# Performance work log

Hardware: AMD Instinct MI355X
Metric: run time of the kernel (lower is better)

## Reference

```python
import jax, jax.numpy as jnp
import numpy as np
from jax import lax


def _conv(x, w, b, pad):
    # NCHW conv with OIHW weights, stride 1, symmetric padding.
    y = lax.conv_general_dilated(
        x, w, window_strides=(1, 1), padding=[(pad, pad), (pad, pad)],
        dimension_numbers=("NCHW", "OIHW", "NCHW"))
    return y + b[None, :, None, None]


def setup_inputs() -> dict:
    key = jax.random.key(0)
    ks = jax.random.split(key, 12)
    B, H, W = 8, 96, 128
    CORR = 324  # 4 * (2*4+1)^2
    return {
        "flow": jax.random.normal(ks[0], (B, 2, H, W), jnp.float32),
        "corr": jax.random.normal(ks[1], (B, CORR, H, W), jnp.float32),
        "wc1": jax.random.normal(ks[2], (256, CORR, 1, 1), jnp.float32) * 0.05,
        "bc1": jax.random.normal(ks[3], (256,), jnp.float32) * 0.05,
        "wc2": jax.random.normal(ks[4], (192, 256, 3, 3), jnp.float32) * 0.05,
        "bc2": jax.random.normal(ks[5], (192,), jnp.float32) * 0.05,
        "wf1": jax.random.normal(ks[6], (128, 2, 7, 7), jnp.float32) * 0.05,
        "bf1": jax.random.normal(ks[7], (128,), jnp.float32) * 0.05,
        "wf2": jax.random.normal(ks[8], (64, 128, 3, 3), jnp.float32) * 0.05,
        "bf2": jax.random.normal(ks[9], (64,), jnp.float32) * 0.05,
        "wo": jax.random.normal(ks[10], (126, 256, 3, 3), jnp.float32) * 0.05,
        "bo": jax.random.normal(ks[11], (126,), jnp.float32) * 0.05,
    }


def reference(flow, corr, wc1, bc1, wc2, bc2, wf1, bf1, wf2, bf2, wo, bo):
    # All DeformConv2d layers run with zero offsets -> standard convs.
    cor = jax.nn.relu(_conv(corr, wc1, bc1, 0))        # [B,256,H,W]
    cor = jax.nn.relu(_conv(cor, wc2, bc2, 1))         # [B,192,H,W]
    flo = jax.nn.relu(_conv(flow, wf1, bf1, 3))        # [B,128,H,W]
    flo = jax.nn.relu(_conv(flo, wf2, bf2, 1))         # [B,64,H,W]
    cor_flo = jnp.concatenate([cor, flo], axis=1)      # [B,256,H,W]
    out = jax.nn.relu(_conv(cor_flo, wo, bo, 1))       # [B,126,H,W]
    return jnp.concatenate([out, flow], axis=1)        # [B,128,H,W]
```

## Files before the change

kernel.cpp:

```cpp
#include <hip/hip_runtime.h>


typedef __bf16 bf16x8 __attribute__((ext_vector_type(8)));
typedef float f32x4 __attribute__((ext_vector_type(4)));

__device__ __forceinline__ unsigned short f2bf(float f) {
  __bf16 h = (__bf16)f;
  return __builtin_bit_cast(unsigned short, h);
}
__device__ __forceinline__ float bf2f(unsigned short u) {
  __bf16 h = __builtin_bit_cast(__bf16, u);
  return (float)h;
}

__device__ __forceinline__ void gload_lds16(const unsigned short* g,
                                            unsigned short* l) {
  __builtin_amdgcn_global_load_lds(
      (const __attribute__((address_space(1))) unsigned int*)g,
      (__attribute__((address_space(3))) unsigned int*)l, 16, 0, 0);
}

__global__ __launch_bounds__(256) void repack_w_bf16(
    const float* __restrict__ w, unsigned short* __restrict__ dst, int O, int I,
    int K2, int ICQ, int OCP) {
  int n = K2 * ICQ * OCP * 8;
  for (int s = blockIdx.x * 256 + threadIdx.x; s < n; s += gridDim.x * 256) {
    int j = s & 7;
    int r = s >> 3;
    int oc = r % OCP;
    r /= OCP;
    int icq = r % ICQ;
    int tap = r / ICQ;
    int ic = icq * 8 + j;
    float v = (oc < O && ic < I) ? w[((size_t)oc * I + ic) * K2 + tap] : 0.f;
    dst[s] = f2bf(v);
  }
}

__global__ __launch_bounds__(256) void repack_wf1(const float* __restrict__ w,
                                                  unsigned short* __restrict__ dst) {
  int s = blockIdx.x * 256 + threadIdx.x;
  if (s >= 16384) return;
  int j = s & 7;
  int oc = (s >> 3) & 127;
  int kq = s >> 10;
  int k = kq * 8 + j;
  float v = 0.f;
  if (k < 98) {
    int ic = k / 49;
    int tap = k - ic * 49;
    v = w[(oc * 2 + ic) * 49 + tap];
  }
  dst[s] = f2bf(v);
}

__global__ __launch_bounds__(256) void nchw2nhwc_bf16(
    const float* __restrict__ in, unsigned short* __restrict__ outp, int C,
    int CP, int HW) {
  __shared__ float sls[64][65];
  int p0 = blockIdx.x * 64;
  int c0 = blockIdx.y * 64;
  int b = p0 / HW, hw0 = p0 % HW;
  int tid = threadIdx.x;
  for (int e = tid; e < 4096; e += 256) {
    int ch = e >> 6, px = e & 63;
    float v = 0.f;
    if (c0 + ch < C) v = in[(size_t)(b * C + c0 + ch) * HW + hw0 + px];
    sls[px][ch] = v;
  }
  __syncthreads();
  for (int e = tid; e < 512; e += 256) {
    int px = e >> 3, cc = e & 7;
    if (c0 + cc * 8 < CP) {
      unsigned short pk[8];
#pragma unroll
      for (int j = 0; j < 8; ++j) pk[j] = f2bf(sls[px][cc * 8 + j]);
      *(uint4*)&outp[(size_t)(p0 + px) * CP + c0 + cc * 8] = *(uint4*)pk;
    }
  }
}

__global__ __launch_bounds__(256) void nhwc_bf16_2nchw(
    const unsigned short* __restrict__ inp, float* __restrict__ outp, int CP,
    int CO, int CT, int HW) {
  __shared__ float sls[64][65];
  int p0 = blockIdx.x * 64, c0 = blockIdx.y * 64;
  int b = p0 / HW, hw0 = p0 % HW;
  int tid = threadIdx.x;
  for (int e = tid; e < 512; e += 256) {
    int px = e >> 3, cc = e & 7;
    uint4 v = *(const uint4*)&inp[(size_t)(p0 + px) * CP + c0 + cc * 8];
    unsigned short* ps = (unsigned short*)&v;
#pragma unroll
    for (int j = 0; j < 8; ++j) sls[px][cc * 8 + j] = bf2f(ps[j]);
  }
  __syncthreads();
  for (int e = tid; e < 1024; e += 256) {
    int ch = e >> 4, pq = e & 15;
    if (c0 + ch < CO) {
      float4 v;
      v.x = sls[pq * 4 + 0][ch];
      v.y = sls[pq * 4 + 1][ch];
      v.z = sls[pq * 4 + 2][ch];
      v.w = sls[pq * 4 + 3][ch];
      *(float4*)&outp[(size_t)(b * CT + c0 + ch) * HW + hw0 + pq * 4] = v;
    }
  }
}

__global__ __launch_bounds__(256) void zero_halo3(unsigned short* b0,
                                                  unsigned short* b1,
                                                  unsigned short* b2) {
  unsigned short* buf = (blockIdx.y == 0) ? b0 : (blockIdx.y == 1) ? b1 : b2;
  const int C = (blockIdx.y == 2) ? 128 : 256;
  const int cq = C >> 3;
  int n = 8 * 452 * cq;
  int i = blockIdx.x * 256 + threadIdx.x;
  if (i >= n) return;
  int c = i % cq;
  int t = i / cq;
  int bp = t % 452;
  int bb = t / 452;
  int y, x;
  if (bp < 130) { y = 0; x = bp; }
  else if (bp < 260) { y = 97; x = bp - 130; }
  else { int r = bp - 260; y = 1 + (r >> 1); x = (r & 1) ? 129 : 0; }
  *(uint4*)&buf[((size_t)(bb * 98 + y) * 130 + x) * C + c * 8] =
      make_uint4(0, 0, 0, 0);
}

__global__ __launch_bounds__(256) void im2col_flow(const float* __restrict__ f,
                                                   unsigned short* __restrict__ o,
                                                   int H, int W) {
  int s = blockIdx.x * 256 + threadIdx.x;
  int kq = s & 15;
  int px = s >> 4;
  int HW = H * W;
  int b = px / HW;
  int r = px % HW;
  int y = r / W;
  int x = r % W;
  unsigned short pk[8];
#pragma unroll
  for (int j = 0; j < 8; ++j) {
    int k = kq * 8 + j;
    float v = 0.f;
    if (k < 98) {
      int ic = k / 49;
      int t = k - ic * 49;
      int dy = t / 7, dx = t - dy * 7;
      int yy = y + dy - 3, xx = x + dx - 3;
      if (yy >= 0 && yy < H && xx >= 0 && xx < W)
        v = f[((size_t)(b * 2 + ic) * H + yy) * W + xx];
    }
    pk[j] = f2bf(v);
  }
  *(uint4*)&o[(size_t)px * 128 + kq * 8] = *(uint4*)pk;
}

template <int CINP, int NF>
__global__ __launch_bounds__(256, 2) void mfma_gemm(
    const unsigned short* __restrict__ xin,
    const unsigned short* __restrict__ wpk,
    const float* __restrict__ bias, unsigned short* __restrict__ yout,
    int H, int W, int Cout, int OCP, int CT, int coff, int Wo, int oh) {
  __shared__ __align__(16) unsigned short smem[NF * 2048];
  const int tid = threadIdx.x;
  const int wave = tid >> 6, lane = tid & 63;
  const int l15 = lane & 15, lq = lane >> 4;
  const int tilesX = W >> 4;
  const int perB = (H >> 4) * tilesX;
  const int b = blockIdx.x / perB;
  const int r0 = blockIdx.x % perB;
  const int ty0 = (r0 / tilesX) << 4;
  const int tx0 = (r0 % tilesX) << 4;
  const int oc0 = blockIdx.y * (NF * 16);

  f32x4 acc[4][NF];
#pragma unroll
  for (int mf = 0; mf < 4; ++mf)
#pragma unroll
    for (int nf = 0; nf < NF; ++nf) acc[mf][nf] = (f32x4){0.f, 0.f, 0.f, 0.f};

  size_t rowA[4];
#pragma unroll
  for (int mf = 0; mf < 4; ++mf)
    rowA[mf] =
        ((size_t)(b * H + ty0 + wave * 4 + mf) * W + tx0 + l15) * CINP + lq * 8;
  const unsigned short* wB = wpk + ((size_t)lq * OCP + oc0 + l15) * 8;
  const int icbStr = 4 * OCP * 8;

  constexpr int NI = CINP / 32;
#pragma unroll 2
  for (int icb = 0; icb < NI; ++icb) {
    bf16x8 va[4], vb[NF];
#pragma unroll
    for (int mf = 0; mf < 4; ++mf)
      va[mf] = *(const bf16x8*)&xin[rowA[mf] + icb * 32];
#pragma unroll
    for (int nf = 0; nf < NF; ++nf)
      vb[nf] = *(const bf16x8*)&wB[icb * icbStr + nf * 128];
    __builtin_amdgcn_s_setprio(1);
#pragma unroll
    for (int mf = 0; mf < 4; ++mf)
#pragma unroll
      for (int nf = 0; nf < NF; ++nf)
        acc[mf][nf] = __builtin_amdgcn_mfma_f32_16x16x32_bf16(
            va[mf], vb[nf], acc[mf][nf], 0, 0, 0);
    __builtin_amdgcn_s_setprio(0);
  }

  float bsv[NF];
#pragma unroll
  for (int nf = 0; nf < NF; ++nf) {
    int oc = oc0 + nf * 16 + l15;
    bsv[nf] = (oc < Cout) ? bias[oc] : 0.f;
  }
  unsigned short* slice = smem + wave * (NF * 512);
  const int Ho = H + 2 * oh;
#pragma unroll
  for (int pass = 0; pass < 2; ++pass) {
#pragma unroll
    for (int mf = 0; mf < 4; ++mf)
#pragma unroll
      for (int h = 0; h < NF / 2; ++h) {
        const int nf = pass * (NF / 2) + h;
#pragma unroll
        for (int r = 0; r < 4; ++r)
          slice[(mf * 16 + lq * 4 + r) * (NF * 8) + h * 16 + l15] =
              f2bf(fmaxf(acc[mf][nf][r] + bsv[nf], 0.f));
      }
#pragma unroll
    for (int j = 0; j < NF; ++j) {
      int c = j * 64 + lane;
      int pxl = c / NF;
      int ocq = (c - pxl * NF) * 8;
      uint4 v = *(uint4*)&slice[pxl * (NF * 8) + ocq];
      int pxg = wave * 64 + pxl;
      int gy = ty0 + (pxg >> 4) + oh, gx = tx0 + (pxg & 15) + oh;
      *(uint4*)&yout[((size_t)(b * Ho + gy) * Wo + gx) * CT + coff + oc0 +
                     pass * (NF * 8) + ocq] = v;
    }
  }
}

template <int CINP, int NF>
__global__ __launch_bounds__(256, 2) void mfma_conv3(
    const unsigned short* __restrict__ xin,
    const unsigned short* __restrict__ wpk,
    const float* __restrict__ bias, unsigned short* __restrict__ yout,
    int H, int W, int Cout, int OCP, int CT, int coff, int Wo, int oh) {
  const int Hp = H + 2, Wp = W + 2;
  constexpr int ICQS = CINP / 8;
  constexpr int NI = CINP / 32;
  __shared__ __align__(16) unsigned short smem[24576];

  const int tid = threadIdx.x;
  const int wave = tid >> 6, lane = tid & 63;
  const int l15 = lane & 15, lq = lane >> 4;
  const int tilesX = W >> 4;
  const int perB = (H >> 4) * tilesX;
  const int b = blockIdx.x / perB;
  const int r0 = blockIdx.x % perB;
  const int ty0 = (r0 / tilesX) << 4;
  const int tx0 = (r0 % tilesX) << 4;
  const int oc0 = blockIdx.y * (NF * 16);

  f32x4 acc[4][NF];
#pragma unroll
  for (int mf = 0; mf < 4; ++mf)
#pragma unroll
    for (int nf = 0; nf < NF; ++nf) acc[mf][nf] = (f32x4){0.f, 0.f, 0.f, 0.f};

  const size_t rowbase = (size_t)(b * Hp + ty0) * Wp + tx0;
  const unsigned short* gp[6];
#pragma unroll
  for (int k = 0; k < 6; ++k) {
    int e = tid + k * 256;
    int q = e / 384;
    int r = e - q * 384;
    int rc = (r < 324) ? r : 323;
    int py = rc / 18, px = rc - py * 18;
    gp[k] = xin + (rowbase + (size_t)py * Wp + px) * CINP + q * 8;
  }
  const unsigned short* wB = wpk + ((size_t)lq * OCP + oc0 + l15) * 8;
  const int icbStr = 4 * OCP * 8;
  const int tapStr = ICQS * OCP * 8;

#pragma unroll
  for (int k = 0; k < 6; ++k)
    gload_lds16(gp[k], smem + (tid + k * 256) * 8);

  for (int icb = 0; icb < NI; ++icb) {
    const int curOff = (icb & 1) * 12288;
    __syncthreads();
    if (icb + 1 < NI) {
      const int nxtOff = curOff ^ 12288;
#pragma unroll
      for (int k = 0; k < 6; ++k)
        gload_lds16(gp[k] + (icb + 1) * 32,
                    smem + nxtOff + (tid + k * 256) * 8);
    }
    const unsigned short* wbi = wB + icb * icbStr;
#pragma unroll
    for (int tap = 0; tap < 9; ++tap) {
      const int dy = tap / 3, dx = tap - dy * 3;
      bf16x8 vb[NF], va[4];
#pragma unroll
      for (int nf = 0; nf < NF; ++nf)
        vb[nf] = *(const bf16x8*)&wbi[tap * tapStr + nf * 128];
#pragma unroll
      for (int mf = 0; mf < 4; ++mf)
        va[mf] = *(const bf16x8*)
            &smem[curOff +
                  (lq * 384 + (wave * 4 + mf + dy) * 18 + l15 + dx) * 8];
      __builtin_amdgcn_s_setprio(1);
#pragma unroll
      for (int mf = 0; mf < 4; ++mf)
#pragma unroll
        for (int nf = 0; nf < NF; ++nf)
          acc[mf][nf] = __builtin_amdgcn_mfma_f32_16x16x32_bf16(
              va[mf], vb[nf], acc[mf][nf], 0, 0, 0);
      __builtin_amdgcn_s_setprio(0);
    }
  }
  __syncthreads();

  float bsv[NF];
#pragma unroll
  for (int nf = 0; nf < NF; ++nf) {
    int oc = oc0 + nf * 16 + l15;
    bsv[nf] = (oc < Cout) ? bias[oc] : 0.f;
  }
  unsigned short* slice = smem + wave * (NF * 512);
  const int Ho = H + 2 * oh;
#pragma unroll
  for (int pass = 0; pass < 2; ++pass) {
#pragma unroll
    for (int mf = 0; mf < 4; ++mf)
#pragma unroll
      for (int h = 0; h < NF / 2; ++h) {
        const int nf = pass * (NF / 2) + h;
#pragma unroll
        for (int r = 0; r < 4; ++r)
          slice[(mf * 16 + lq * 4 + r) * (NF * 8) + h * 16 + l15] =
              f2bf(fmaxf(acc[mf][nf][r] + bsv[nf], 0.f));
      }
#pragma unroll
    for (int j = 0; j < NF; ++j) {
      int c = j * 64 + lane;
      int pxl = c / NF;
      int ocq = (c - pxl * NF) * 8;
      uint4 v = *(uint4*)&slice[pxl * (NF * 8) + ocq];
      int pxg = wave * 64 + pxl;
      int gy = ty0 + (pxg >> 4) + oh, gx = tx0 + (pxg & 15) + oh;
      *(uint4*)&yout[((size_t)(b * Ho + gy) * Wo + gx) * CT + coff + oc0 +
                     pass * (NF * 8) + ocq] = v;
    }
  }
}

__global__ __launch_bounds__(256) void copy_flow(const float* __restrict__ flow,
                                                 float* __restrict__ out, int B,
                                                 int HW) {
  int q = HW / 4;
  int n = B * 2 * q;
  int i = blockIdx.x * blockDim.x + threadIdx.x;
  if (i < n) {
    float4 v = ((const float4*)flow)[i];
    int p = i % q;
    int t = i / q;
    int c = t % 2;
    int bb = t / 2;
    ((float4*)out)[((bb * 128 + 126 + c) * HW) / 4 + p] = v;
  }
}

extern "C" void kernel_launch(void* const* d_in, const int* in_sizes, int n_in,
                              void* d_out, int out_size, void* d_ws,
                              size_t ws_size, hipStream_t stream) {
  const float* flow = (const float*)d_in[0];
  const float* corr = (const float*)d_in[1];
  const float* wc1 = (const float*)d_in[2];
  const float* bc1 = (const float*)d_in[3];
  const float* wc2 = (const float*)d_in[4];
  const float* bc2 = (const float*)d_in[5];
  const float* wf1 = (const float*)d_in[6];
  const float* bf1 = (const float*)d_in[7];
  const float* wf2 = (const float*)d_in[8];
  const float* bf2 = (const float*)d_in[9];
  const float* wo = (const float*)d_in[10];
  const float* bo = (const float*)d_in[11];
  float* out = (float*)d_out;

  const int B = 8, H = 96, W = 128;
  const int HW = H * W;
  const size_t NPX = (size_t)B * HW;

  char* ws = (char*)d_ws;
  unsigned short* corrT = (unsigned short*)(ws + 0);
  unsigned short* cat = (unsigned short*)(ws + 0);
  unsigned short* buf1 = (unsigned short*)(ws + 69206016);
  unsigned short* fcol = (unsigned short*)(ws + 69206016);
  unsigned short* out5 = (unsigned short*)(ws + 69206016 + 25165824);
  unsigned short* flo1 = (unsigned short*)(ws + 121389056);
  unsigned short* p1 = (unsigned short*)(ws + 147480576);
  unsigned short* p2 = (unsigned short*)(ws + 147660800);
  unsigned short* p3 = (unsigned short*)(ws + 148545536);
  unsigned short* p4 = (unsigned short*)(ws + 148692992);
  unsigned short* pf1 = (unsigned short*)(ws + 149282816);

  repack_w_bf16<<<dim3(128), dim3(256), 0, stream>>>(wc1, p1, 256, 324, 1, 44, 256);
  repack_w_bf16<<<dim3(256), dim3(256), 0, stream>>>(wc2, p2, 192, 256, 9, 32, 192);
  repack_w_bf16<<<dim3(64), dim3(256), 0, stream>>>(wf2, p3, 64, 128, 9, 16, 64);
  repack_w_bf16<<<dim3(192), dim3(256), 0, stream>>>(wo, p4, 126, 256, 9, 32, 128);
  repack_wf1<<<dim3(64), dim3(256), 0, stream>>>(wf1, pf1);

  nchw2nhwc_bf16<<<dim3(NPX / 64, 6), dim3(256), 0, stream>>>(corr, corrT, 324,
                                                              352, HW);
  mfma_gemm<352, 8><<<dim3(384, 2), dim3(256), 0, stream>>>(
      corrT, p1, bc1, buf1, H, W, 256, 256, 256, 0, 130, 1);
  zero_halo3<<<dim3(512, 3), dim3(256), 0, stream>>>(buf1, cat, flo1);
  mfma_conv3<256, 6><<<dim3(384, 2), dim3(256), 0, stream>>>(
      buf1, p2, bc2, cat, H, W, 192, 192, 256, 0, 130, 1);
  im2col_flow<<<dim3(NPX * 16 / 256), dim3(256), 0, stream>>>(flow, fcol, H, W);
  mfma_gemm<128, 8><<<dim3(384, 1), dim3(256), 0, stream>>>(
      fcol, pf1, bf1, flo1, H, W, 128, 128, 128, 0, 130, 1);
  mfma_conv3<128, 4><<<dim3(384, 1), dim3(256), 0, stream>>>(
      flo1, p3, bf2, cat, H, W, 64, 64, 256, 192, 130, 1);
  mfma_conv3<256, 8><<<dim3(384, 1), dim3(256), 0, stream>>>(
      cat, p4, bo, out5, H, W, 126, 128, 128, 0, 128, 0);
  nhwc_bf16_2nchw<<<dim3(NPX / 64, 2), dim3(256), 0, stream>>>(out5, out, 128,
                                                               126, 128, HW);
  copy_flow<<<dim3(192), dim3(256), 0, stream>>>(flow, out, B, HW);
}
```

Baseline: 532.3 us.

## Fuse layout transposes into conv kernels and merge prep launches

The first 1x1 GEMM now reads the NCHW fp32 corr tensor directly, converting it to bf16 and transposing it into LDS with a register-prefetch double buffer. This removes the separate NCHW-to-NHWC transpose pass and its intermediate buffer. The final conv writes fp32 NCHW output straight from its accumulators, removing the bf16 output buffer and the transpose-back kernel. The weight repacks and halo zeroing are merged into one multi-task launch to cut launch count. The trade-off is that the strided per-channel global reads in the GEMM and the scattered float4 stores in the last conv may coalesce less well than the dedicated transpose kernels did.

Result: slower. 764.7 us (+43.7%).

```diff
diff --git a/kernel.cpp b/kernel.cpp
--- a/kernel.cpp
+++ b/kernel.cpp
@@ -7,10 +7,6 @@
 __device__ __forceinline__ unsigned short f2bf(float f) {
   __bf16 h = (__bf16)f;
   return __builtin_bit_cast(unsigned short, h);
-}
-__device__ __forceinline__ float bf2f(unsigned short u) {
-  __bf16 h = __builtin_bit_cast(__bf16, u);
-  return (float)h;
 }
 
 __device__ __forceinline__ void gload_lds16(const unsigned short* g,
@@ -20,113 +16,69 @@
       (__attribute__((address_space(3))) unsigned int*)l, 16, 0, 0);
 }
 
-__global__ __launch_bounds__(256) void repack_w_bf16(
-    const float* __restrict__ w, unsigned short* __restrict__ dst, int O, int I,
-    int K2, int ICQ, int OCP) {
-  int n = K2 * ICQ * OCP * 8;
-  for (int s = blockIdx.x * 256 + threadIdx.x; s < n; s += gridDim.x * 256) {
-    int j = s & 7;
-    int r = s >> 3;
-    int oc = r % OCP;
-    r /= OCP;
-    int icq = r % ICQ;
-    int tap = r / ICQ;
-    int ic = icq * 8 + j;
-    float v = (oc < O && ic < I) ? w[((size_t)oc * I + ic) * K2 + tap] : 0.f;
-    dst[s] = f2bf(v);
-  }
-}
-
-__global__ __launch_bounds__(256) void repack_wf1(const float* __restrict__ w,
-                                                  unsigned short* __restrict__ dst) {
-  int s = blockIdx.x * 256 + threadIdx.x;
-  if (s >= 16384) return;
-  int j = s & 7;
-  int oc = (s >> 3) & 127;
-  int kq = s >> 10;
-  int k = kq * 8 + j;
-  float v = 0.f;
-  if (k < 98) {
-    int ic = k / 49;
-    int tap = k - ic * 49;
-    v = w[(oc * 2 + ic) * 49 + tap];
-  }
-  dst[s] = f2bf(v);
-}
-
-__global__ __launch_bounds__(256) void nchw2nhwc_bf16(
-    const float* __restrict__ in, unsigned short* __restrict__ outp, int C,
-    int CP, int HW) {
-  __shared__ float sls[64][65];
-  int p0 = blockIdx.x * 64;
-  int c0 = blockIdx.y * 64;
-  int b = p0 / HW, hw0 = p0 % HW;
-  int tid = threadIdx.x;
-  for (int e = tid; e < 4096; e += 256) {
-    int ch = e >> 6, px = e & 63;
-    float v = 0.f;
-    if (c0 + ch < C) v = in[(size_t)(b * C + c0 + ch) * HW + hw0 + px];
-    sls[px][ch] = v;
-  }
-  __syncthreads();
-  for (int e = tid; e < 512; e += 256) {
-    int px = e >> 3, cc = e & 7;
-    if (c0 + cc * 8 < CP) {
-      unsigned short pk[8];
-#pragma unroll
-      for (int j = 0; j < 8; ++j) pk[j] = f2bf(sls[px][cc * 8 + j]);
-      *(uint4*)&outp[(size_t)(p0 + px) * CP + c0 + cc * 8] = *(uint4*)pk;
-    }
-  }
-}
-
-__global__ __launch_bounds__(256) void nhwc_bf16_2nchw(
-    const unsigned short* __restrict__ inp, float* __restrict__ outp, int CP,
-    int CO, int CT, int HW) {
-  __shared__ float sls[64][65];
-  int p0 = blockIdx.x * 64, c0 = blockIdx.y * 64;
-  int b = p0 / HW, hw0 = p0 % HW;
-  int tid = threadIdx.x;
-  for (int e = tid; e < 512; e += 256) {
-    int px = e >> 3, cc = e & 7;
-    uint4 v = *(const uint4*)&inp[(size_t)(p0 + px) * CP + c0 + cc * 8];
-    unsigned short* ps = (unsigned short*)&v;
-#pragma unroll
-    for (int j = 0; j < 8; ++j) sls[px][cc * 8 + j] = bf2f(ps[j]);
-  }
-  __syncthreads();
-  for (int e = tid; e < 1024; e += 256) {
-    int ch = e >> 4, pq = e & 15;
-    if (c0 + ch < CO) {
-      float4 v;
-      v.x = sls[pq * 4 + 0][ch];
-      v.y = sls[pq * 4 + 1][ch];
-      v.z = sls[pq * 4 + 2][ch];
-      v.w = sls[pq * 4 + 3][ch];
-      *(float4*)&outp[(size_t)(b * CT + c0 + ch) * HW + hw0 + pq * 4] = v;
-    }
-  }
-}
-
-__global__ __launch_bounds__(256) void zero_halo3(unsigned short* b0,
-                                                  unsigned short* b1,
-                                                  unsigned short* b2) {
-  unsigned short* buf = (blockIdx.y == 0) ? b0 : (blockIdx.y == 1) ? b1 : b2;
-  const int C = (blockIdx.y == 2) ? 128 : 256;
-  const int cq = C >> 3;
-  int n = 8 * 452 * cq;
-  int i = blockIdx.x * 256 + threadIdx.x;
-  if (i >= n) return;
-  int c = i % cq;
-  int t = i / cq;
-  int bp = t % 452;
-  int bb = t / 452;
-  int y, x;
-  if (bp < 130) { y = 0; x = bp; }
-  else if (bp < 260) { y = 97; x = bp - 130; }
-  else { int r = bp - 260; y = 1 + (r >> 1); x = (r & 1) ? 129 : 0; }
-  *(uint4*)&buf[((size_t)(bb * 98 + y) * 130 + x) * C + c * 8] =
-      make_uint4(0, 0, 0, 0);
+__global__ __launch_bounds__(256) void prep(
+    const float* __restrict__ wc1, const float* __restrict__ wc2,
+    const float* __restrict__ wf2, const float* __restrict__ wo,
+    const float* __restrict__ wf1, unsigned short* __restrict__ p1,
+    unsigned short* __restrict__ p2, unsigned short* __restrict__ p3,
+    unsigned short* __restrict__ p4, unsigned short* __restrict__ pf1,
+    unsigned short* __restrict__ hb0, unsigned short* __restrict__ hb1,
+    unsigned short* __restrict__ hb2) {
+  const int task = blockIdx.y;
+  const int tid0 = blockIdx.x * 256 + threadIdx.x;
+  if (task < 4) {
+    const float* w;
+    unsigned short* dst;
+    int O, I, K2, ICQ, OCP;
+    if (task == 0) { w = wc1; dst = p1; O = 256; I = 324; K2 = 1;  ICQ = 44; OCP = 256; }
+    else if (task == 1) { w = wc2; dst = p2; O = 192; I = 256; K2 = 9; ICQ = 32; OCP = 192; }
+    else if (task == 2) { w = wf2; dst = p3; O = 64;  I = 128; K2 = 9; ICQ = 16; OCP = 64; }
+    else { w = wo; dst = p4; O = 126; I = 256; K2 = 9; ICQ = 32; OCP = 128; }
+    int n = K2 * ICQ * OCP * 8;
+    for (int s = tid0; s < n; s += gridDim.x * 256) {
+      int j = s & 7;
+      int r = s >> 3;
+      int oc = r % OCP;
+      r /= OCP;
+      int icq = r % ICQ;
+      int tap = r / ICQ;
+      int ic = icq * 8 + j;
+      float v = (oc < O && ic < I) ? w[((size_t)oc * I + ic) * K2 + tap] : 0.f;
+      dst[s] = f2bf(v);
+    }
+  } else if (task == 4) {
+    int s = tid0;
+    if (s < 16384) {
+      int j = s & 7;
+      int oc = (s >> 3) & 127;
+      int kq = s >> 10;
+      int k = kq * 8 + j;
+      float v = 0.f;
+      if (k < 98) {
+        int ic = k / 49;
+        int tap = k - ic * 49;
+        v = wf1[(oc * 2 + ic) * 49 + tap];
+      }
+      pf1[s] = f2bf(v);
+    }
+  } else {
+    unsigned short* buf = (task == 5) ? hb0 : (task == 6) ? hb1 : hb2;
+    const int C = (task == 7) ? 128 : 256;
+    const int cq = C >> 3;
+    int n = 8 * 452 * cq;
+    int i = tid0;
+    if (i >= n) return;
+    int c = i % cq;
+    int t = i / cq;
+    int bp = t % 452;
+    int bb = t / 452;
+    int y, x;
+    if (bp < 130) { y = 0; x = bp; }
+    else if (bp < 260) { y = 97; x = bp - 130; }
+    else { int r = bp - 260; y = 1 + (r >> 1); x = (r & 1) ? 129 : 0; }
+    *(uint4*)&buf[((size_t)(bb * 98 + y) * 130 + x) * C + c * 8] =
+        make_uint4(0, 0, 0, 0);
+  }
 }
 
 __global__ __launch_bounds__(256) void im2col_flow(const float* __restrict__ f,
@@ -244,11 +196,136 @@
   }
 }
 
-template <int CINP, int NF>
+template <int NF>
+__global__ __launch_bounds__(256, 2) void mfma_gemm_nchw(
+    const float* __restrict__ xin,
+    const unsigned short* __restrict__ wpk,
+    const float* __restrict__ bias, unsigned short* __restrict__ yout,
+    int H, int W, int Cout, int OCP, int CT, int coff, int Wo, int oh) {
+  constexpr int NI = 11;
+  __shared__ __align__(16) unsigned short smem[16384];
+  const int tid = threadIdx.x;
+  const int wave = tid >> 6, lane = tid & 63;
+  const int l15 = lane & 15, lq = lane >> 4;
+  const int HW = H * W;
+  const int tilesX = W >> 4;
+  const int perB = (H >> 4) * tilesX;
+  const int b = blockIdx.x / perB;
+  const int r0 = blockIdx.x % perB;
+  const int ty0 = (r0 / tilesX) << 4;
+  const int tx0 = (r0 % tilesX) << 4;
+  const int oc0 = blockIdx.y * (NF * 16);
+
+  f32x4 acc[4][NF];
+#pragma unroll
+  for (int mf = 0; mf < 4; ++mf)
+#pragma unroll
+    for (int nf = 0; nf < NF; ++nf) acc[mf][nf] = (f32x4){0.f, 0.f, 0.f, 0.f};
+
+  const unsigned short* wB = wpk + ((size_t)lq * OCP + oc0 + l15) * 8;
+  const int icbStr = 4 * OCP * 8;
+  const float* gsrc =
+      xin + (size_t)b * 324 * HW + (size_t)(ty0 + lq) * W + tx0 + l15;
+
+  float ld[32];
+#pragma unroll
+  for (int j = 0; j < 8; ++j) {
+    int ch = wave * 8 + j;
+    const float* cp = gsrc + (size_t)ch * HW;
+#pragma unroll
+    for (int p = 0; p < 4; ++p) ld[j * 4 + p] = cp[p * 4 * W];
+  }
+#pragma unroll
+  for (int p = 0; p < 4; ++p) {
+    unsigned short pk[8];
+#pragma unroll
+    for (int j = 0; j < 8; ++j) pk[j] = f2bf(ld[j * 4 + p]);
+    *(uint4*)&smem[(wave * 256 + lane + p * 64) * 8] = *(uint4*)pk;
+  }
+
+  for (int icb = 0; icb < NI; ++icb) {
+    __syncthreads();
+    const int curOff = (icb & 1) * 8192;
+    const bool have = (icb + 1 < NI);
+    if (have) {
+#pragma unroll
+      for (int j = 0; j < 8; ++j) {
+        int ch = (icb + 1) * 32 + wave * 8 + j;
+        const float* cp = gsrc + (size_t)ch * HW;
+        bool ok = ch < 324;
+#pragma unroll
+        for (int p = 0; p < 4; ++p) ld[j * 4 + p] = ok ? cp[p * 4 * W] : 0.f;
+      }
+    }
+    bf16x8 va[4], vb[NF];
+    const unsigned short* wbi = wB + (size_t)icb * icbStr;
+#pragma unroll
+    for (int nf = 0; nf < NF; ++nf) vb[nf] = *(const bf16x8*)&wbi[nf * 128];
+#pragma unroll
+    for (int mf = 0; mf < 4; ++mf)
+      va[mf] = *(const bf16x8*)
+          &smem[curOff + (lq * 256 + (wave * 4 + mf) * 16 + l15) * 8];
+    __builtin_amdgcn_s_setprio(1);
+#pragma unroll
+    for (int mf = 0; mf < 4; ++mf)
+#pragma unroll
+      for (int nf = 0; nf < NF; ++nf)
+        acc[mf][nf] = __builtin_amdgcn_mfma_f32_16x16x32_bf16(
+            va[mf], vb[nf], acc[mf][nf], 0, 0, 0);
+    __builtin_amdgcn_s_setprio(0);
+    if (have) {
+      const int nxtOff = curOff ^ 8192;
+#pragma unroll
+      for (int p = 0; p < 4; ++p) {
+        unsigned short pk[8];
+#pragma unroll
+        for (int j = 0; j < 8; ++j) pk[j] = f2bf(ld[j * 4 + p]);
+        *(uint4*)&smem[nxtOff + (wave * 256 + lane + p * 64) * 8] =
+            *(uint4*)pk;
+      }
+    }
+  }
+  __syncthreads();
+
+  float bsv[NF];
+#pragma unroll
+  for (int nf = 0; nf < NF; ++nf) {
+    int oc = oc0 + nf * 16 + l15;
+    bsv[nf] = (oc < Cout) ? bias[oc] : 0.f;
+  }
+  unsigned short* slice = smem + wave * (NF * 512);
+  const int Ho = H + 2 * oh;
+#pragma unroll
+  for (int pass = 0; pass < 2; ++pass) {
+#pragma unroll
+    for (int mf = 0; mf < 4; ++mf)
+#pragma unroll
+      for (int h = 0; h < NF / 2; ++h) {
+        const int nf = pass * (NF / 2) + h;
+#pragma unroll
+        for (int r = 0; r < 4; ++r)
+          slice[(mf * 16 + lq * 4 + r) * (NF * 8) + h * 16 + l15] =
+              f2bf(fmaxf(acc[mf][nf][r] + bsv[nf], 0.f));
+      }
+#pragma unroll
+    for (int j = 0; j < NF; ++j) {
+      int c = j * 64 + lane;
+      int pxl = c / NF;
+      int ocq = (c - pxl * NF) * 8;
+      uint4 v = *(uint4*)&slice[pxl * (NF * 8) + ocq];
+      int pxg = wave * 64 + pxl;
+      int gy = ty0 + (pxg >> 4) + oh, gx = tx0 + (pxg & 15) + oh;
+      *(uint4*)&yout[((size_t)(b * Ho + gy) * Wo + gx) * CT + coff + oc0 +
+                     pass * (NF * 8) + ocq] = v;
+    }
+  }
+}
+
+template <int CINP, int NF, bool F32OUT>
 __global__ __launch_bounds__(256, 2) void mfma_conv3(
     const unsigned short* __restrict__ xin,
     const unsigned short* __restrict__ wpk,
-    const float* __restrict__ bias, unsigned short* __restrict__ yout,
+    const float* __restrict__ bias, void* __restrict__ yout,
     int H, int W, int Cout, int OCP, int CT, int coff, int Wo, int oh) {
   const int Hp = H + 2, Wp = W + 2;
   constexpr int ICQS = CINP / 8;
@@ -326,36 +403,60 @@
   }
   __syncthreads();
 
-  float bsv[NF];
-#pragma unroll
-  for (int nf = 0; nf < NF; ++nf) {
-    int oc = oc0 + nf * 16 + l15;
-    bsv[nf] = (oc < Cout) ? bias[oc] : 0.f;
-  }
-  unsigned short* slice = smem + wave * (NF * 512);
-  const int Ho = H + 2 * oh;
-#pragma unroll
-  for (int pass = 0; pass < 2; ++pass) {
-#pragma unroll
-    for (int mf = 0; mf < 4; ++mf)
-#pragma unroll
-      for (int h = 0; h < NF / 2; ++h) {
-        const int nf = pass * (NF / 2) + h;
-#pragma unroll
-        for (int r = 0; r < 4; ++r)
-          slice[(mf * 16 + lq * 4 + r) * (NF * 8) + h * 16 + l15] =
-              f2bf(fmaxf(acc[mf][nf][r] + bsv[nf], 0.f));
-      }
-#pragma unroll
-    for (int j = 0; j < NF; ++j) {
-      int c = j * 64 + lane;
-      int pxl = c / NF;
-      int ocq = (c - pxl * NF) * 8;
-      uint4 v = *(uint4*)&slice[pxl * (NF * 8) + ocq];
-      int pxg = wave * 64 + pxl;
-      int gy = ty0 + (pxg >> 4) + oh, gx = tx0 + (pxg & 15) + oh;
-      *(uint4*)&yout[((size_t)(b * Ho + gy) * Wo + gx) * CT + coff + oc0 +
+  if constexpr (F32OUT) {
+    float* op = (float*)yout;
+#pragma unroll
+    for (int nf = 0; nf < NF; ++nf) {
+      int oc = oc0 + nf * 16 + l15;
+      if (oc < Cout) {
+        float bv = bias[oc];
+#pragma unroll
+        for (int mf = 0; mf < 4; ++mf) {
+          float4 v;
+          v.x = fmaxf(acc[mf][nf][0] + bv, 0.f);
+          v.y = fmaxf(acc[mf][nf][1] + bv, 0.f);
+          v.z = fmaxf(acc[mf][nf][2] + bv, 0.f);
+          v.w = fmaxf(acc[mf][nf][3] + bv, 0.f);
+          *(float4*)&op[((size_t)(b * CT + coff + oc) * H + ty0 + wave * 4 +
+                         mf) *
+                            W +
+                        tx0 + lq * 4] = v;
+        }
+      }
+    }
+  } else {
+    unsigned short* yo = (unsigned short*)yout;
+    float bsv[NF];
+#pragma unroll
+    for (int nf = 0; nf < NF; ++nf) {
+      int oc = oc0 + nf * 16 + l15;
+      bsv[nf] = (oc < Cout) ? bias[oc] : 0.f;
+    }
+    unsigned short* slice = smem + wave * (NF * 512);
+    const int Ho = H + 2 * oh;
+#pragma unroll
+    for (int pass = 0; pass < 2; ++pass) {
+#pragma unroll
+      for (int mf = 0; mf < 4; ++mf)
+#pragma unroll
+        for (int h = 0; h < NF / 2; ++h) {
+          const int nf = pass * (NF / 2) + h;
+#pragma unroll
+          for (int r = 0; r < 4; ++r)
+            slice[(mf * 16 + lq * 4 + r) * (NF * 8) + h * 16 + l15] =
+                f2bf(fmaxf(acc[mf][nf][r] + bsv[nf], 0.f));
+        }
+#pragma unroll
+      for (int j = 0; j < NF; ++j) {
+        int c = j * 64 + lane;
+        int pxl = c / NF;
+        int ocq = (c - pxl * NF) * 8;
+        uint4 v = *(uint4*)&slice[pxl * (NF * 8) + ocq];
+        int pxg = wave * 64 + pxl;
+        int gy = ty0 + (pxg >> 4) + oh, gx = tx0 + (pxg & 15) + oh;
+        *(uint4*)&yo[((size_t)(b * Ho + gy) * Wo + gx) * CT + coff + oc0 +
                      pass * (NF * 8) + ocq] = v;
+      }
     }
   }
 }
@@ -398,11 +499,9 @@
   const size_t NPX = (size_t)B * HW;
 
   char* ws = (char*)d_ws;
-  unsigned short* corrT = (unsigned short*)(ws + 0);
   unsigned short* cat = (unsigned short*)(ws + 0);
   unsigned short* buf1 = (unsigned short*)(ws + 69206016);
   unsigned short* fcol = (unsigned short*)(ws + 69206016);
-  unsigned short* out5 = (unsigned short*)(ws + 69206016 + 25165824);
   unsigned short* flo1 = (unsigned short*)(ws + 121389056);
   unsigned short* p1 = (unsigned short*)(ws + 147480576);
   unsigned short* p2 = (unsigned short*)(ws + 147660800);
@@ -410,27 +509,18 @@
   unsigned short* p4 = (unsigned short*)(ws + 148692992);
   unsigned short* pf1 = (unsigned short*)(ws + 149282816);
 
-  repack_w_bf16<<<dim3(128), dim3(256), 0, stream>>>(wc1, p1, 256, 324, 1, 44, 256);
-  repack_w_bf16<<<dim3(256), dim3(256), 0, stream>>>(wc2, p2, 192, 256, 9, 32, 192);
-  repack_w_bf16<<<dim3(64), dim3(256), 0, stream>>>(wf2, p3, 64, 128, 9, 16, 64);
-  repack_w_bf16<<<dim3(192), dim3(256), 0, stream>>>(wo, p4, 126, 256, 9, 32, 128);
-  repack_wf1<<<dim3(64), dim3(256), 0, stream>>>(wf1, pf1);
-
-  nchw2nhwc_bf16<<<dim3(NPX / 64, 6), dim3(256), 0, stream>>>(corr, corrT, 324,
-                                                              352, HW);
-  mfma_gemm<352, 8><<<dim3(384, 2), dim3(256), 0, stream>>>(
-      corrT, p1, bc1, buf1, H, W, 256, 256, 256, 0, 130, 1);
-  zero_halo3<<<dim3(512, 3), dim3(256), 0, stream>>>(buf1, cat, flo1);
-  mfma_conv3<256, 6><<<dim3(384, 2), dim3(256), 0, stream>>>(
-      buf1, p2, bc2, cat, H, W, 192, 192, 256, 0, 130, 1);
+  prep<<<dim3(512, 8), dim3(256), 0, stream>>>(wc1, wc2, wf2, wo, wf1, p1, p2,
+                                               p3, p4, pf1, buf1, cat, flo1);
+  mfma_gemm_nchw<8><<<dim3(384, 2), dim3(256), 0, stream>>>(
+      corr, p1, bc1, buf1, H, W, 256, 256, 256, 0, 130, 1);
+  mfma_conv3<256, 6, false><<<dim3(384, 2), dim3(256), 0, stream>>>(
+      buf1, p2, bc2, (void*)cat, H, W, 192, 192, 256, 0, 130, 1);
   im2col_flow<<<dim3(NPX * 16 / 256), dim3(256), 0, stream>>>(flow, fcol, H, W);
   mfma_gemm<128, 8><<<dim3(384, 1), dim3(256), 0, stream>>>(
       fcol, pf1, bf1, flo1, H, W, 128, 128, 128, 0, 130, 1);
-  mfma_conv3<128, 4><<<dim3(384, 1), dim3(256), 0, stream>>>(
-      flo1, p3, bf2, cat, H, W, 64, 64, 256, 192, 130, 1);
-  mfma_conv3<256, 8><<<dim3(384, 1), dim3(256), 0, stream>>>(
-      cat, p4, bo, out5, H, W, 126, 128, 128, 0, 128, 0);
-  nhwc_bf16_2nchw<<<dim3(NPX / 64, 2), dim3(256), 0, stream>>>(out5, out, 128,
-                                                               126, 128, HW);
+  mfma_conv3<128, 4, false><<<dim3(384, 1), dim3(256), 0, stream>>>(
+      flo1, p3, bf2, (void*)cat, H, W, 64, 64, 256, 192, 130, 1);
+  mfma_conv3<256, 8, true><<<dim3(384, 1), dim3(256), 0, stream>>>(
+      cat, p4, bo, (void*)out, H, W, 126, 128, 128, 0, 128, 0);
   copy_flow<<<dim3(192), dim3(256), 0, stream>>>(flow, out, B, HW);
 }
```
